# Performance work log

Hardware: AMD Instinct MI355X
Metric: run time of the kernel (lower is better)

## Reference

```python
import jax, jax.numpy as jnp
import numpy as np

DIM = 1024
CTX_DIM = 768

def setup_inputs() -> dict:
    key = jax.random.key(0)
    ks = jax.random.split(key, 12)
    B, Sq, Skv = 8, 2048, 2048
    s_d = 1.0 / np.sqrt(DIM)
    s_c = 1.0 / np.sqrt(CTX_DIM)
    return {
        "x": jax.random.normal(ks[0], (B, Sq, DIM), jnp.float32),
        "context": jax.random.normal(ks[1], (B, Skv, CTX_DIM), jnp.float32),
        # nn.Linear weights are [out_features, in_features]
        "Wq": jax.random.uniform(ks[2], (DIM, DIM), jnp.float32, -s_d, s_d),
        "bq": jax.random.uniform(ks[3], (DIM,), jnp.float32, -s_d, s_d),
        "Wk": jax.random.uniform(ks[4], (DIM, CTX_DIM), jnp.float32, -s_c, s_c),
        "bk": jax.random.uniform(ks[5], (DIM,), jnp.float32, -s_c, s_c),
        "Wv": jax.random.uniform(ks[6], (DIM, CTX_DIM), jnp.float32, -s_c, s_c),
        "bv": jax.random.uniform(ks[7], (DIM,), jnp.float32, -s_c, s_c),
        "Wo": jax.random.uniform(ks[8], (DIM, DIM), jnp.float32, -s_d, s_d),
        "bo": jax.random.uniform(ks[9], (DIM,), jnp.float32, -s_d, s_d),
    }

def reference(x, context, Wq, bq, Wk, bk, Wv, bv, Wo, bo):
    # q: [B,Sq,D], k,v: [B,Skv,D]
    q = jnp.einsum('bsi,di->bsd', x, Wq) + bq
    k = jnp.einsum('bsc,dc->bsd', context, Wk) + bk
    v = jnp.einsum('bsc,dc->bsd', context, Wv) + bv
    scale = 1.0 / jnp.sqrt(jnp.asarray(q.shape[-1], q.dtype))
    scores = jnp.einsum('bqd,bkd->bqk', q, k) * scale  # [B,Sq,Skv]
    att = jax.nn.softmax(scores, axis=-1)
    out = jnp.einsum('bqk,bkd->bqd', att, v)
    return jnp.einsum('bqd,od->bqo', out, Wo) + bo
```

## Files before the change

### kernel.cpp

```cpp
#include <hip/hip_runtime.h>

typedef unsigned short u16;
typedef unsigned int   u32;
typedef __attribute__((ext_vector_type(8))) short short8;
typedef __attribute__((ext_vector_type(4))) float f32x4;

#define DIM   1024
#define CDIM  768
#define BATCH 8
#define SQ    2048
#define SKV   2048

__device__ __forceinline__ u16 f2bf(float f) {
    union { float f; u32 u; } c; c.f = f;
    u32 u = c.u;
    u += 0x7fffu + ((u >> 16) & 1u);
    return (u16)(u >> 16);
}

__device__ __forceinline__ void async_copy16(const u16* g, u16* l) {
    __builtin_amdgcn_global_load_lds(
        (const __attribute__((address_space(1))) void*)g,
        (__attribute__((address_space(3))) void*)l,
        16, 0, 0);
}

__device__ __forceinline__ void cvt4(const float* s, u16* d, int i) {
    float4 f = ((const float4*)s)[i];
    ushort4 o;
    o.x = f2bf(f.x); o.y = f2bf(f.y); o.z = f2bf(f.z); o.w = f2bf(f.w);
    ((ushort4*)d)[i] = o;
}

__global__ __launch_bounds__(256)
void conv_xc(const float* __restrict__ x, const float* __restrict__ ctx,
             u16* __restrict__ dx, u16* __restrict__ dc)
{
    int i = blockIdx.x * 256 + threadIdx.x;
    if (i < 4194304) cvt4(x, dx, i);
    else             cvt4(ctx, dc, i - 4194304);
}

__global__ __launch_bounds__(256)
void conv_w(const float* __restrict__ Wq, const float* __restrict__ Wk,
            const float* __restrict__ Wv, const float* __restrict__ Wo,
            u16* __restrict__ dq, u16* __restrict__ dk,
            u16* __restrict__ dv, u16* __restrict__ dw)
{
    int i = blockIdx.x * 256 + threadIdx.x;
    if      (i < 262144) cvt4(Wq, dq, i);
    else if (i < 458752) cvt4(Wk, dk, i - 262144);
    else if (i < 655360) cvt4(Wv, dv, i - 458752);
    else                 cvt4(Wo, dw, i - 655360);
}

template<int BIAS_MODE, int OUT_MODE>
__global__ __launch_bounds__(256, 2)
void gemm_nt(const u16* __restrict__ A, int lda, long sA,
             const u16* __restrict__ Bw, int ldb, long sB,
             const float* __restrict__ bias,
             void* __restrict__ Cout, int ldc, long sC,
             int K, float scale, float* __restrict__ lsum)
{
    __shared__ u16 As[128 * 64];
    __shared__ u16 Bs[128 * 64];
    const int t    = threadIdx.x;
    const int lane = t & 63;
    const int w    = t >> 6;
    const int l15  = lane & 15;
    const int quad = lane >> 4;
    const int wm = w >> 1, wn = w & 1;
    const long m0 = (long)blockIdx.x * 128;
    const long n0 = (long)blockIdx.y * 128;
    A  += (long)blockIdx.z * sA;
    Bw += (long)blockIdx.z * sB;

    const int srow   = lane >> 3;
    const int schunk = (lane & 7) ^ srow;

    const f32x4 fz = {0.f, 0.f, 0.f, 0.f};
    f32x4 acc[4][4];
#pragma unroll
    for (int i = 0; i < 4; ++i)
#pragma unroll
        for (int j = 0; j < 4; ++j) acc[i][j] = fz;

    for (int k0 = 0; k0 < K; k0 += 64) {
#pragma unroll
        for (int j = 0; j < 4; ++j) {
            int rb = w * 32 + j * 8;
            async_copy16(A  + (m0 + rb + srow) * (long)lda + k0 + schunk * 8, &As[rb * 64]);
            async_copy16(Bw + (n0 + rb + srow) * (long)ldb + k0 + schunk * 8, &Bs[rb * 64]);
        }
        __syncthreads();
#pragma unroll
        for (int kc = 0; kc < 2; ++kc) {
            short8 a[4], b[4];
#pragma unroll
            for (int i = 0; i < 4; ++i) {
                int R = wm * 64 + i * 16 + l15;
                a[i] = *(const short8*)&As[R * 64 + (((kc * 4 + quad) ^ (l15 & 7)) * 8)];
            }
#pragma unroll
            for (int j = 0; j < 4; ++j) {
                int R = wn * 64 + j * 16 + l15;
                b[j] = *(const short8*)&Bs[R * 64 + (((kc * 4 + quad) ^ (l15 & 7)) * 8)];
            }
#pragma unroll
            for (int i = 0; i < 4; ++i)
#pragma unroll
                for (int j = 0; j < 4; ++j)
                    acc[i][j] = __builtin_amdgcn_mfma_f32_16x16x32_bf16(a[i], b[j], acc[i][j], 0, 0, 0);
        }
        __syncthreads();
    }

    float invl[4][4];
    if (BIAS_MODE == 3) {
        const long lbase = (long)blockIdx.z * gridDim.x * 128 + m0 + wm * 64;
#pragma unroll
        for (int i = 0; i < 4; ++i)
#pragma unroll
            for (int r = 0; r < 4; ++r)
                invl[i][r] = 1.f / lsum[lbase + i * 16 + quad * 4 + r];
    }

    float rowpart[4][4];
    if (OUT_MODE == 2) {
#pragma unroll
        for (int i = 0; i < 4; ++i)
#pragma unroll
            for (int r = 0; r < 4; ++r) rowpart[i][r] = 0.f;
    }

#pragma unroll
    for (int i = 0; i < 4; ++i) {
#pragma unroll
        for (int j = 0; j < 4; ++j) {
            long n = n0 + wn * 64 + j * 16 + l15;
#pragma unroll
            for (int r = 0; r < 4; ++r) {
                long m = m0 + wm * 64 + i * 16 + quad * 4 + r;
                float v = acc[i][j][r];
                if (BIAS_MODE == 0) v += bias[n];
                else if (BIAS_MODE == 1) v += bias[m];
                v *= scale;
                if (OUT_MODE == 2) { v = __expf(v); rowpart[i][r] += v; }
                if (BIAS_MODE == 3) v *= invl[i][r];
                long off = (long)blockIdx.z * sC + m * (long)ldc + n;
                if (OUT_MODE == 1) ((float*)Cout)[off] = v;
                else               ((u16*)Cout)[off]   = f2bf(v);
            }
        }
    }

    if (OUT_MODE == 2) {
#pragma unroll
        for (int i = 0; i < 4; ++i)
#pragma unroll
            for (int r = 0; r < 4; ++r) {
                float p = rowpart[i][r];
                p += __shfl_xor(p, 1);
                p += __shfl_xor(p, 2);
                p += __shfl_xor(p, 4);
                p += __shfl_xor(p, 8);
                if (l15 == 0)
                    atomicAdd(&lsum[(long)blockIdx.z * gridDim.x * 128 +
                                    m0 + wm * 64 + i * 16 + quad * 4 + r], p);
            }
    }
}

extern "C" void kernel_launch(void* const* d_in, const int* in_sizes, int n_in,
                              void* d_out, int out_size, void* d_ws, size_t ws_size,
                              hipStream_t stream)
{
    const float* x   = (const float*)d_in[0];
    const float* ctx = (const float*)d_in[1];
    const float* Wq  = (const float*)d_in[2];
    const float* bq  = (const float*)d_in[3];
    const float* Wk  = (const float*)d_in[4];
    const float* bk  = (const float*)d_in[5];
    const float* Wv  = (const float*)d_in[6];
    const float* bv  = (const float*)d_in[7];
    const float* Wo  = (const float*)d_in[8];
    const float* bo  = (const float*)d_in[9];

    const int MQ  = BATCH * SQ;
    const int NX  = MQ * DIM;
    const int NC  = MQ * CDIM;
    const int NWQ = DIM * DIM;
    const int NWK = DIM * CDIM;

    u16* ws     = (u16*)d_ws;
    u16* xo_bf  = ws;
    u16* ctx_bf = xo_bf + NX;
    u16* k_bf   = ctx_bf + NC;
    u16* vt_bf  = k_bf + NX;
    u16* wq_bf  = vt_bf + NX;
    u16* wk_bf  = wq_bf + NWQ;
    u16* wv_bf  = wk_bf + NWK;
    u16* wo_bf  = wv_bf + NWK;
    u16* S      = wo_bf + NWQ;
    float* lsum = (float*)(S + (long)MQ * SKV);
    u16* q_bf   = (u16*)d_out;

    hipMemsetAsync(lsum, 0, MQ * sizeof(float), stream);

    conv_xc<<<(NX + NC) / 1024, 256, 0, stream>>>(x, ctx, xo_bf, ctx_bf);
    conv_w<<<(2 * NWQ + 2 * NWK) / 1024, 256, 0, stream>>>(
        Wq, Wk, Wv, Wo, wq_bf, wk_bf, wv_bf, wo_bf);

    gemm_nt<0, 0><<<dim3(MQ / 128, DIM / 128, 1), 256, 0, stream>>>(
        xo_bf, DIM, 0, wq_bf, DIM, 0, bq, q_bf, DIM, 0, DIM, 0.03125f, nullptr);
    gemm_nt<0, 0><<<dim3(MQ / 128, DIM / 128, 1), 256, 0, stream>>>(
        ctx_bf, CDIM, 0, wk_bf, CDIM, 0, bk, k_bf, DIM, 0, CDIM, 1.0f, nullptr);
    gemm_nt<1, 0><<<dim3(DIM / 128, MQ / 128, 1), 256, 0, stream>>>(
        wv_bf, CDIM, 0, ctx_bf, CDIM, 0, bv, vt_bf, MQ, 0, CDIM, 1.0f, nullptr);

    gemm_nt<2, 2><<<dim3(SQ / 128, SKV / 128, BATCH), 256, 0, stream>>>(
        q_bf, DIM, (long)SQ * DIM, k_bf, DIM, (long)SKV * DIM,
        nullptr, S, SKV, (long)SQ * SKV, DIM, 1.0f, lsum);

    gemm_nt<3, 0><<<dim3(SQ / 128, DIM / 128, BATCH), 256, 0, stream>>>(
        S, SKV, (long)SQ * SKV, vt_bf, MQ, (long)SKV,
        nullptr, xo_bf, DIM, (long)SQ * DIM, SKV, 1.0f, lsum);

    gemm_nt<0, 1><<<dim3(MQ / 128, DIM / 128, 1), 256, 0, stream>>>(
        xo_bf, DIM, 0, wo_bf, DIM, 0, bo, d_out, DIM, 0, DIM, 1.0f, nullptr);
}
```

Baseline: 458.6 us.

## Rewrite GEMM as 256x256 tile, 8-wave, double-buffered pipelined kernel

Replaces the 128x128 single-buffered GEMM with a 256x256 tile computed by 512 threads (8 waves), using double-buffered LDS (128 KB) and staged async global-to-LDS loads interleaved with MFMA quarter-blocks. Explicit barriers, waitcnt and setprio are used so loads for the next tile overlap with compute. This removes the load-then-compute serialization and raises data reuse per LDS byte. The cost is large LDS use per block, which limits occupancy, and higher register pressure from the 8x4 accumulators. Fewer blocks may also cause tail imbalance on the smaller projection GEMMs.

Measured after the change: 459.3 us. Within noise of the previous version (+0.2%).

```diff
diff --git a/kernel.cpp b/kernel.cpp
--- a/kernel.cpp
+++ b/kernel.cpp
@@ -54,100 +54,191 @@
     else                 cvt4(Wo, dw, i - 655360);
 }
 
+__device__ __forceinline__ void stage_half(const u16* __restrict__ G, long ld, long k0,
+                                           u16* lbase, int h, int w, int lane)
+{
+    const int srow = lane >> 3;
+    const int sch  = (lane & 7) ^ srow;
+#pragma unroll
+    for (int q = 0; q < 2; ++q) {
+        int rb = h * 128 + q * 64 + w * 8;
+        async_copy16(G + (long)(rb + srow) * ld + k0 + sch * 8, lbase + rb * 64);
+    }
+}
+
+
+#define BARRIER()                                                              \
+    do {                                                                       \
+        asm volatile("" ::: "memory");                                         \
+        __builtin_amdgcn_s_barrier();                                          \
+        asm volatile("" ::: "memory");                                         \
+    } while (0)
+
+#define LOAD_A(Xs, mh)                                                         \
+    do {                                                                       \
+        _Pragma("unroll") for (int kc = 0; kc < 2; ++kc)                       \
+        _Pragma("unroll") for (int i = 0; i < 4; ++i) {                        \
+            int R = wm * 128 + (mh) * 64 + i * 16 + l15;                       \
+            a[kc][i] = *(const short8*)&(Xs)[R * 64 +                          \
+                         (((kc * 4 + quad) ^ (l15 & 7)) * 8)];                 \
+        }                                                                      \
+    } while (0)
+
+#define LOAD_B(Xs, nh, dst)                                                    \
+    do {                                                                       \
+        _Pragma("unroll") for (int kc = 0; kc < 2; ++kc)                       \
+        _Pragma("unroll") for (int j = 0; j < 2; ++j) {                        \
+            int R = wn * 64 + (nh) * 32 + j * 16 + l15;                        \
+            dst[kc][j] = *(const short8*)&(Xs)[R * 64 +                        \
+                         (((kc * 4 + quad) ^ (l15 & 7)) * 8)];                 \
+        }                                                                      \
+    } while (0)
+
+#define MFMA_Q(mh, nh, bb)                                                     \
+    do {                                                                       \
+        _Pragma("unroll") for (int kc = 0; kc < 2; ++kc)                       \
+        _Pragma("unroll") for (int i = 0; i < 4; ++i)                          \
+        _Pragma("unroll") for (int j = 0; j < 2; ++j)                          \
+            acc[(mh) * 4 + i][(nh) * 2 + j] =                                  \
+                __builtin_amdgcn_mfma_f32_16x16x32_bf16(                       \
+                    a[kc][i], bb[kc][j],                                       \
+                    acc[(mh) * 4 + i][(nh) * 2 + j], 0, 0, 0);                 \
+    } while (0)
+
+#define TILE_ITER(CUR, TT)                                                     \
+    do {                                                                       \
+        u16* As = &smem[CUR][0][0];                                            \
+        u16* Bs = &smem[CUR][1][0];                                            \
+        u16* An = &smem[(CUR) ^ 1][0][0];                                      \
+                                                \
+        LOAD_A(As, 0);                                                         \
+        LOAD_B(Bs, 0, b0);                                                     \
+        if ((TT) + 1 < NT)                                                     \
+            stage_half(gA, lda, ((long)(TT) + 1) * 64, An, 0, w, lane);        \
+        BARRIER();                                                             \
+        asm volatile("s_waitcnt lgkmcnt(0)" ::: "memory");                     \
+        __builtin_amdgcn_s_setprio(1);                                         \
+        MFMA_Q(0, 0, b0);                                                      \
+        __builtin_amdgcn_s_setprio(0);                                         \
+        BARRIER();                                                             \
+                                                \
+        LOAD_B(Bs, 1, b1);                                                     \
+        if ((TT) + 1 < NT)                                                     \
+            stage_half(gA, lda, ((long)(TT) + 1) * 64, An, 1, w, lane);        \
+        BARRIER();                                                             \
+        asm volatile("s_waitcnt lgkmcnt(0)" ::: "memory");                     \
+        __builtin_amdgcn_s_setprio(1);                                         \
+        MFMA_Q(0, 1, b1);                                                      \
+        __builtin_amdgcn_s_setprio(0);                                         \
+        BARRIER();                                                             \
+                                                \
+        LOAD_A(As, 1);                                                         \
+        if ((TT) + 2 < NT)                                                     \
+            stage_half(gB, ldb, ((long)(TT) + 2) * 64, Bs, 0, w, lane);        \
+        BARRIER();                                                             \
+        asm volatile("s_waitcnt lgkmcnt(0)" ::: "memory");                     \
+        __builtin_amdgcn_s_setprio(1);                                         \
+        MFMA_Q(1, 0, b0);                                                      \
+        __builtin_amdgcn_s_setprio(0);                                         \
+        BARRIER();                                                             \
+                                                \
+        if ((TT) + 2 < NT) {                                                   \
+            stage_half(gB, ldb, ((long)(TT) + 2) * 64, Bs, 1, w, lane);        \
+            asm volatile("s_waitcnt vmcnt(4)" ::: "memory");                   \
+        } else if ((TT) + 1 < NT) {                                            \
+            asm volatile("s_waitcnt vmcnt(0)" ::: "memory");                   \
+        }                                                                      \
+        __builtin_amdgcn_sched_barrier(0);                                     \
+        BARRIER();                                                             \
+        __builtin_amdgcn_s_setprio(1);                                         \
+        MFMA_Q(1, 1, b1);                                                      \
+        __builtin_amdgcn_s_setprio(0);                                         \
+        BARRIER();                                                             \
+    } while (0)
+
 template<int BIAS_MODE, int OUT_MODE>
-__global__ __launch_bounds__(256, 2)
-void gemm_nt(const u16* __restrict__ A, int lda, long sA,
-             const u16* __restrict__ Bw, int ldb, long sB,
+__global__ __launch_bounds__(512, 2)
+void gemm_nt(const u16* __restrict__ A, int lda_, long sA,
+             const u16* __restrict__ Bw, int ldb_, long sB,
              const float* __restrict__ bias,
-             void* __restrict__ Cout, int ldc, long sC,
+             void* __restrict__ Cout, int ldc_, long sC,
              int K, float scale, float* __restrict__ lsum)
 {
-    __shared__ u16 As[128 * 64];
-    __shared__ u16 Bs[128 * 64];
+    __shared__ u16 smem[2][2][256 * 64];
     const int t    = threadIdx.x;
     const int lane = t & 63;
     const int w    = t >> 6;
+    const int wm   = w >> 2;
+    const int wn   = w & 3;
     const int l15  = lane & 15;
     const int quad = lane >> 4;
-    const int wm = w >> 1, wn = w & 1;
-    const long m0 = (long)blockIdx.x * 128;
-    const long n0 = (long)blockIdx.y * 128;
-    A  += (long)blockIdx.z * sA;
-    Bw += (long)blockIdx.z * sB;
-
-    const int srow   = lane >> 3;
-    const int schunk = (lane & 7) ^ srow;
-
+    const long lda = lda_, ldb = ldb_, ldc = ldc_;
+    const long m0 = (long)blockIdx.x * 256;
+    const long n0 = (long)blockIdx.y * 256;
+    const u16* gA = A  + (long)blockIdx.z * sA + m0 * lda;
+    const u16* gB = Bw + (long)blockIdx.z * sB + n0 * ldb;
+    const int NT = K >> 6;
+
+    short8 a[2][4], b0[2][2], b1[2][2];
     const f32x4 fz = {0.f, 0.f, 0.f, 0.f};
-    f32x4 acc[4][4];
-#pragma unroll
-    for (int i = 0; i < 4; ++i)
+    f32x4 acc[8][4];
+#pragma unroll
+    for (int i = 0; i < 8; ++i)
 #pragma unroll
         for (int j = 0; j < 4; ++j) acc[i][j] = fz;
 
-    for (int k0 = 0; k0 < K; k0 += 64) {
-#pragma unroll
-        for (int j = 0; j < 4; ++j) {
-            int rb = w * 32 + j * 8;
-            async_copy16(A  + (m0 + rb + srow) * (long)lda + k0 + schunk * 8, &As[rb * 64]);
-            async_copy16(Bw + (n0 + rb + srow) * (long)ldb + k0 + schunk * 8, &Bs[rb * 64]);
-        }
-        __syncthreads();
-#pragma unroll
-        for (int kc = 0; kc < 2; ++kc) {
-            short8 a[4], b[4];
-#pragma unroll
-            for (int i = 0; i < 4; ++i) {
-                int R = wm * 64 + i * 16 + l15;
-                a[i] = *(const short8*)&As[R * 64 + (((kc * 4 + quad) ^ (l15 & 7)) * 8)];
-            }
-#pragma unroll
-            for (int j = 0; j < 4; ++j) {
-                int R = wn * 64 + j * 16 + l15;
-                b[j] = *(const short8*)&Bs[R * 64 + (((kc * 4 + quad) ^ (l15 & 7)) * 8)];
-            }
-#pragma unroll
-            for (int i = 0; i < 4; ++i)
-#pragma unroll
-                for (int j = 0; j < 4; ++j)
-                    acc[i][j] = __builtin_amdgcn_mfma_f32_16x16x32_bf16(a[i], b[j], acc[i][j], 0, 0, 0);
-        }
-        __syncthreads();
-    }
-
-    float invl[4][4];
+    stage_half(gA, lda, 0, &smem[0][0][0], 0, w, lane);
+    stage_half(gA, lda, 0, &smem[0][0][0], 1, w, lane);
+    stage_half(gB, ldb, 0, &smem[0][1][0], 0, w, lane);
+    stage_half(gB, ldb, 0, &smem[0][1][0], 1, w, lane);
+    if (NT > 1) {
+        stage_half(gB, ldb, 64, &smem[1][1][0], 0, w, lane);
+        stage_half(gB, ldb, 64, &smem[1][1][0], 1, w, lane);
+        asm volatile("s_waitcnt vmcnt(4)" ::: "memory");
+    } else {
+        asm volatile("s_waitcnt vmcnt(0)" ::: "memory");
+    }
+    __builtin_amdgcn_sched_barrier(0);
+    BARRIER();
+
+    for (int T = 0; T < NT; T += 2) {
+        TILE_ITER(0, T);
+        TILE_ITER(1, T + 1);
+    }
+
+    float invl[8][4];
     if (BIAS_MODE == 3) {
-        const long lbase = (long)blockIdx.z * gridDim.x * 128 + m0 + wm * 64;
-#pragma unroll
-        for (int i = 0; i < 4; ++i)
+        const long lbase = (long)blockIdx.z * (long)gridDim.x * 256 + m0 + wm * 128;
+#pragma unroll
+        for (int mi = 0; mi < 8; ++mi)
 #pragma unroll
             for (int r = 0; r < 4; ++r)
-                invl[i][r] = 1.f / lsum[lbase + i * 16 + quad * 4 + r];
-    }
-
-    float rowpart[4][4];
+                invl[mi][r] = 1.f / lsum[lbase + mi * 16 + quad * 4 + r];
+    }
+
+    float rowpart[8][4];
     if (OUT_MODE == 2) {
 #pragma unroll
-        for (int i = 0; i < 4; ++i)
-#pragma unroll
-            for (int r = 0; r < 4; ++r) rowpart[i][r] = 0.f;
-    }
-
-#pragma unroll
-    for (int i = 0; i < 4; ++i) {
-#pragma unroll
-        for (int j = 0; j < 4; ++j) {
-            long n = n0 + wn * 64 + j * 16 + l15;
+        for (int mi = 0; mi < 8; ++mi)
+#pragma unroll
+            for (int r = 0; r < 4; ++r) rowpart[mi][r] = 0.f;
+    }
+
+#pragma unroll
+    for (int mi = 0; mi < 8; ++mi) {
+#pragma unroll
+        for (int nj = 0; nj < 4; ++nj) {
+            long n = n0 + wn * 64 + nj * 16 + l15;
 #pragma unroll
             for (int r = 0; r < 4; ++r) {
-                long m = m0 + wm * 64 + i * 16 + quad * 4 + r;
-                float v = acc[i][j][r];
+                long m = m0 + wm * 128 + mi * 16 + quad * 4 + r;
+                float v = acc[mi][nj][r];
                 if (BIAS_MODE == 0) v += bias[n];
                 else if (BIAS_MODE == 1) v += bias[m];
                 v *= scale;
-                if (OUT_MODE == 2) { v = __expf(v); rowpart[i][r] += v; }
-                if (BIAS_MODE == 3) v *= invl[i][r];
-                long off = (long)blockIdx.z * sC + m * (long)ldc + n;
+                if (OUT_MODE == 2) { v = __expf(v); rowpart[mi][r] += v; }
+                if (BIAS_MODE == 3) v *= invl[mi][r];
+                long off = (long)blockIdx.z * sC + m * ldc + n;
                 if (OUT_MODE == 1) ((float*)Cout)[off] = v;
                 else               ((u16*)Cout)[off]   = f2bf(v);
             }
@@ -156,17 +247,17 @@
 
     if (OUT_MODE == 2) {
 #pragma unroll
-        for (int i = 0; i < 4; ++i)
+        for (int mi = 0; mi < 8; ++mi)
 #pragma unroll
             for (int r = 0; r < 4; ++r) {
-                float p = rowpart[i][r];
+                float p = rowpart[mi][r];
                 p += __shfl_xor(p, 1);
                 p += __shfl_xor(p, 2);
                 p += __shfl_xor(p, 4);
                 p += __shfl_xor(p, 8);
                 if (l15 == 0)
-                    atomicAdd(&lsum[(long)blockIdx.z * gridDim.x * 128 +
-                                    m0 + wm * 64 + i * 16 + quad * 4 + r], p);
+                    atomicAdd(&lsum[(long)blockIdx.z * (long)gridDim.x * 256 +
+                                    m0 + wm * 128 + mi * 16 + quad * 4 + r], p);
             }
     }
 }
@@ -211,21 +302,21 @@
     conv_w<<<(2 * NWQ + 2 * NWK) / 1024, 256, 0, stream>>>(
         Wq, Wk, Wv, Wo, wq_bf, wk_bf, wv_bf, wo_bf);
 
-    gemm_nt<0, 0><<<dim3(MQ / 128, DIM / 128, 1), 256, 0, stream>>>(
+    gemm_nt<0, 0><<<dim3(MQ / 256, DIM / 256, 1), 512, 0, stream>>>(
         xo_bf, DIM, 0, wq_bf, DIM, 0, bq, q_bf, DIM, 0, DIM, 0.03125f, nullptr);
-    gemm_nt<0, 0><<<dim3(MQ / 128, DIM / 128, 1), 256, 0, stream>>>(
+    gemm_nt<0, 0><<<dim3(MQ / 256, DIM / 256, 1), 512, 0, stream>>>(
         ctx_bf, CDIM, 0, wk_bf, CDIM, 0, bk, k_bf, DIM, 0, CDIM, 1.0f, nullptr);
-    gemm_nt<1, 0><<<dim3(DIM / 128, MQ / 128, 1), 256, 0, stream>>>(
+    gemm_nt<1, 0><<<dim3(DIM / 256, MQ / 256, 1), 512, 0, stream>>>(
         wv_bf, CDIM, 0, ctx_bf, CDIM, 0, bv, vt_bf, MQ, 0, CDIM, 1.0f, nullptr);
 
-    gemm_nt<2, 2><<<dim3(SQ / 128, SKV / 128, BATCH), 256, 0, stream>>>(
+    gemm_nt<2, 2><<<dim3(SQ / 256, SKV / 256, BATCH), 512, 0, stream>>>(
         q_bf, DIM, (long)SQ * DIM, k_bf, DIM, (long)SKV * DIM,
         nullptr, S, SKV, (long)SQ * SKV, DIM, 1.0f, lsum);
 
-    gemm_nt<3, 0><<<dim3(SQ / 128, DIM / 128, BATCH), 256, 0, stream>>>(
+    gemm_nt<3, 0><<<dim3(SQ / 256, DIM / 256, BATCH), 512, 0, stream>>>(
         S, SKV, (long)SQ * SKV, vt_bf, MQ, (long)SKV,
         nullptr, xo_bf, DIM, (long)SQ * DIM, SKV, 1.0f, lsum);
 
-    gemm_nt<0, 1><<<dim3(MQ / 128, DIM / 128, 1), 256, 0, stream>>>(
+    gemm_nt<0, 1><<<dim3(MQ / 256, DIM / 256, 1), 512, 0, stream>>>(
         xo_bf, DIM, 0, wo_bf, DIM, 0, bo, d_out, DIM, 0, DIM, 1.0f, nullptr);
 }
```
